# Kernel tuning notes

Measured on AMD Instinct MI355X. Metric: run time of the kernel, lower is better.

The kernel has to match this reference:

```python
import jax, jax.numpy as jnp
import numpy as np

N = 100_000       # nodes
E = 1_600_000     # edges
G = 128           # graphs in batch
RAW_ND, RAW_ED = 9, 3
ND, ED, H = 16, 2, 32  # node_dim, edge_dim, GAT hidden (heads=1)


def _p(key, shape, scale=0.1):
    return jax.random.normal(key, shape, dtype=jnp.float32) * scale


def setup_inputs() -> dict:
    key = jax.random.key(0)
    ks = jax.random.split(key, 32)
    inp = {
        "node_feat": jax.random.normal(ks[0], (N, RAW_ND), dtype=jnp.float32),
        "edge_index": jax.random.randint(ks[1], (2, E), 0, N, dtype=jnp.int64)
        if jax.config.jax_enable_x64 else jax.random.randint(ks[1], (2, E), 0, N).astype(jnp.int32),
        "edge_attr": jax.random.normal(ks[2], (E, RAW_ED), dtype=jnp.float32),
        "batch": jnp.sort(jax.random.randint(ks[3], (N,), 0, G)).astype(jnp.int32),
        # encoders
        "W_ne": _p(ks[4], (RAW_ND, ND)), "b_ne": jnp.zeros((ND,), jnp.float32),
        "W_ee": _p(ks[5], (RAW_ED, ED)), "b_ee": jnp.zeros((ED,), jnp.float32),
        # readout
        "W_l3": _p(ks[6], (3 * H, 1)), "b_l3": jnp.zeros((1,), jnp.float32),
    }
    dims_in = [ND, H, H]
    for i in range(3):
        k = jax.random.split(ks[7 + i], 6)
        inp[f"W{i}"] = _p(k[0], (dims_in[i], H))
        inp[f"as{i}"] = _p(k[1], (H,))
        inp[f"ad{i}"] = _p(k[2], (H,))
        inp[f"We{i}"] = _p(k[3], (ED, H))
        inp[f"ae{i}"] = _p(k[4], (H,))
        inp[f"bb{i}"] = jnp.zeros((H,), jnp.float32)
    return inp


def _segment_softmax(logits, seg, num_segments):
    m = jax.ops.segment_max(logits, seg, num_segments=num_segments)
    m = jnp.where(jnp.isfinite(m), m, 0.0)
    e = jnp.exp(logits - m[seg])
    s = jax.ops.segment_sum(e, seg, num_segments=num_segments)
    return e / (s[seg] + 1e-16)


def _gat(x, src, dst, ef, W, a_s, a_d, We, a_e, b):
    # PyG GATConv, heads=1, negative_slope=0.2
    h = x @ W                                   # [N', H]
    a_src = h @ a_s                             # [N']
    a_dst = h @ a_d
    a_edge = (ef @ We) @ a_e                    # [E']
    logits = jax.nn.leaky_relu(a_src[src] + a_dst[dst] + a_edge, 0.2)
    att = _segment_softmax(logits, dst, h.shape[0])
    out = jax.ops.segment_sum(h[src] * att[:, None], dst, num_segments=h.shape[0])
    return out + b


def reference(node_feat, edge_index, edge_attr, batch,
              W_ne, b_ne, W_ee, b_ee, W_l3, b_l3,
              W0, as0, ad0, We0, ae0, bb0,
              W1, as1, ad1, We1, ae1, bb1,
              W2, as2, ad2, We2, ae2, bb2):
    n = node_feat.shape[0]
    x = node_feat @ W_ne + b_ne                 # NodeEncoder -> [N,16]
    ef = edge_attr @ W_ee + b_ee                # EdgeEncoder -> [E,2]
    # add_self_loops=True with fill_value='mean' (PyG default when edge_dim set)
    loop = jnp.arange(n, dtype=edge_index.dtype)
    src = jnp.concatenate([edge_index[0], loop])
    dst = jnp.concatenate([edge_index[1], loop])
    ef_fill = jnp.broadcast_to(ef.mean(axis=0), (n, ef.shape[1]))
    ef_aug = jnp.concatenate([ef, ef_fill], axis=0)
    x1 = _gat(x, src, dst, ef_aug, W0, as0, ad0, We0, ae0, bb0)
    x2 = _gat(x1, src, dst, ef_aug, W1, as1, ad1, We1, ae1, bb1)
    x3 = _gat(x2, src, dst, ef_aug, W2, as2, ad2, We2, ae2, bb2)
    x_cat = jnp.concatenate([x1, x2, x3], axis=1)  # [N, 96]
    sums = jax.ops.segment_sum(x_cat, batch, num_segments=G)
    cnt = jax.ops.segment_sum(jnp.ones((n,), x_cat.dtype), batch, num_segments=G)
    pooled = sums / jnp.maximum(cnt, 1.0)[:, None]   # global mean pool [G,96]
    return pooled @ W_l3 + b_l3                      # [G,1]
```

## Files before the change

### kernel.cpp

```cpp
#include <hip/hip_runtime.h>
#include <hip/hip_fp16.h>


#define NBUCK_SHIFT 8
#define NBUCK_MAX 512
#define CAP 6144
#define SLF_BIT 0x00800000u

__global__ void k_pre(const int* __restrict__ ei1, int* __restrict__ bucket_cnt,
                      const int* __restrict__ batch, int* __restrict__ bounds,
                      const float* __restrict__ Wne, const float* __restrict__ bne,
                      const float* __restrict__ W0, float* __restrict__ wf,
                      int n, int e, int ep, int nbH) {
    int b = blockIdx.x, t = threadIdx.x;
    if (b < nbH) {
        __shared__ int lh[NBUCK_MAX];
        lh[t] = 0; lh[t + 256] = 0;
        __syncthreads();
        int base = b * 4096;
#pragma unroll
        for (int i = 0; i < 16; ++i) {
            int gid = base + i * 256 + t;
            if (gid < ep) {
                int d = (gid < e) ? ei1[gid] : gid - e;
                atomicAdd(&lh[d >> NBUCK_SHIFT], 1);
            }
        }
        __syncthreads();
        if (lh[t]) atomicAdd(&bucket_cnt[t], lh[t]);
        if (lh[t + 256]) atomicAdd(&bucket_cnt[t + 256], lh[t + 256]);
        return;
    }
    for (int i = t; i < 288; i += 256) {
        int m = i >> 5, j = i & 31;
        float a = 0.f;
        for (int k = 0; k < 16; ++k) a += Wne[m * 16 + k] * W0[k * 32 + j];
        wf[i] = a;
    }
    if (t < 32) {
        float a = 0.f;
        for (int k = 0; k < 16; ++k) a += bne[k] * W0[k * 32 + t];
        wf[288 + t] = a;
    }
    for (int g = t; g <= 128; g += 256) {
        if (g == 128) { bounds[128] = n; continue; }
        int lo = 0, hi = n;
        while (lo < hi) {
            int mid = (lo + hi) >> 1;
            if (batch[mid] < g) lo = mid + 1; else hi = mid;
        }
        bounds[g] = lo;
    }
}

__global__ void k_hproj0(const float* __restrict__ nf, const float* __restrict__ wf,
                         const float* __restrict__ as_, const float* __restrict__ ad_,
                         unsigned int* __restrict__ h2, float* __restrict__ asrc,
                         float* __restrict__ adst, int n) {
    int node = blockIdx.x * 8 + (threadIdx.x >> 5);
    int j = threadIdx.x & 31;
    if (node >= n) return;
    const float* xr = nf + node * 9;
    float acc = wf[288 + j];
#pragma unroll
    for (int m = 0; m < 9; ++m) acc += xr[m] * wf[m * 32 + j];
    float accp = __shfl_down(acc, 1, 32);
    if ((j & 1) == 0) {
        __half2 hh = __floats2half2_rn(acc, accp);
        h2[(size_t)node * 16 + (j >> 1)] = *reinterpret_cast<unsigned int*>(&hh);
    }
    float r1 = acc * as_[j], r2 = acc * ad_[j];
#pragma unroll
    for (int off = 16; off > 0; off >>= 1) {
        r1 += __shfl_xor(r1, off, 32);
        r2 += __shfl_xor(r2, off, 32);
    }
    if (j == 0) { asrc[node] = r1; adst[node] = r2; }
}

__device__ __forceinline__ float2 h2f2u(unsigned int hw) {
    __half2 hh = *reinterpret_cast<__half2*>(&hw);
    return make_float2(__low2float(hh), __high2float(hh));
}

__global__ void k_hproj(const unsigned int* __restrict__ xh, const float* __restrict__ W,
                        const float* __restrict__ as_, const float* __restrict__ ad_,
                        unsigned int* __restrict__ h2, float* __restrict__ asrc,
                        float* __restrict__ adst, int n) {
    __shared__ float sW[1024];
    for (int i = threadIdx.x; i < 1024; i += 256) sW[i] = W[i];
    __syncthreads();
    int node = blockIdx.x * 8 + (threadIdx.x >> 5);
    int j = threadIdx.x & 31;
    if (node >= n) return;
    const unsigned int* xr = xh + (size_t)node * 16;
    float acc = 0.f;
#pragma unroll
    for (int w = 0; w < 16; ++w) {
        float2 f = h2f2u(xr[w]);
        acc += f.x * sW[(2 * w) * 32 + j] + f.y * sW[(2 * w + 1) * 32 + j];
    }
    float accp = __shfl_down(acc, 1, 32);
    if ((j & 1) == 0) {
        __half2 hh = __floats2half2_rn(acc, accp);
        h2[(size_t)node * 16 + (j >> 1)] = *reinterpret_cast<unsigned int*>(&hh);
    }
    float r1 = acc * as_[j], r2 = acc * ad_[j];
#pragma unroll
    for (int off = 16; off > 0; off >>= 1) {
        r1 += __shfl_xor(r1, off, 32);
        r2 += __shfl_xor(r2, off, 32);
    }
    if (j == 0) { asrc[node] = r1; adst[node] = r2; }
}

__global__ void __launch_bounds__(512)
k_scan(const int* __restrict__ bucket_cnt, int* __restrict__ bucket_base,
       int* __restrict__ bcursor, int nbuck, int ep, int* __restrict__ rp, int n) {
    __shared__ int s[512];
    int t = threadIdx.x;
    int v = (t < nbuck) ? bucket_cnt[t] : 0;
    s[t] = v;
    __syncthreads();
    for (int o = 1; o < 512; o <<= 1) {
        int x = (t >= o) ? s[t - o] : 0;
        __syncthreads();
        s[t] += x;
        __syncthreads();
    }
    int ex = s[t] - v;
    if (t < nbuck) { bucket_base[t] = ex; bcursor[t] = ex; }
    if (t == 0) { bucket_base[nbuck] = ep; rp[n] = ep; }
}

__global__ void k_binB(const int* __restrict__ ei0, const int* __restrict__ ei1,
                       const float* __restrict__ ea, const float* __restrict__ We,
                       const float* __restrict__ be, int* __restrict__ bcursor,
                       uint2* __restrict__ st, float2* __restrict__ partial,
                       int e, int ep) {
    __shared__ int lh[NBUCK_MAX], lcur[NBUCK_MAX];
    int t = threadIdx.x;
    lh[t] = 0; lh[t + 256] = 0;
    __syncthreads();
    int base = blockIdx.x * 4096;
    unsigned int sd[16], fh[16];
    int bk[16];
    float w00 = We[0], w10 = We[2], w20 = We[4];
    float w01 = We[1], w11 = We[3], w21 = We[5];
    float b0 = be[0], b1 = be[1];
    float cs0 = 0.f, cs1 = 0.f;
#pragma unroll
    for (int i = 0; i < 16; ++i) {
        int gid = base + i * 256 + t;
        bk[i] = -1;
        if (gid < ep) {
            int s, d;
            if (gid < e) {
                s = ei0[gid]; d = ei1[gid];
                const float* r = ea + (size_t)gid * 3;
                float a0 = r[0], a1 = r[1], a2 = r[2];
                float f0 = a0 * w00 + a1 * w10 + a2 * w20 + b0;
                float f1 = a0 * w01 + a1 * w11 + a2 * w21 + b1;
                cs0 += f0; cs1 += f1;
                sd[i] = ((unsigned int)s << NBUCK_SHIFT) | (unsigned int)(d & 255);
                __half2 hh = __floats2half2_rn(f0, f1);
                fh[i] = *reinterpret_cast<unsigned int*>(&hh);
            } else {
                s = d = gid - e;
                sd[i] = 0x80000000u | ((unsigned int)s << NBUCK_SHIFT)
                      | (unsigned int)(d & 255);
                fh[i] = 0;
            }
            bk[i] = d >> NBUCK_SHIFT;
            atomicAdd(&lh[bk[i]], 1);
        }
    }
#pragma unroll
    for (int off = 32; off > 0; off >>= 1) {
        cs0 += __shfl_xor(cs0, off, 64);
        cs1 += __shfl_xor(cs1, off, 64);
    }
    if ((t & 63) == 0)
        partial[(blockIdx.x << 2) + (t >> 6)] = make_float2(cs0, cs1);
    __syncthreads();
    if (lh[t] > 0) lcur[t] = atomicAdd(&bcursor[t], lh[t]);
    if (lh[t + 256] > 0) lcur[t + 256] = atomicAdd(&bcursor[t + 256], lh[t + 256]);
    __syncthreads();
#pragma unroll
    for (int i = 0; i < 16; ++i) {
        if (bk[i] >= 0) {
            int pos = atomicAdd(&lcur[bk[i]], 1);
            st[pos] = make_uint2(sd[i], fh[i]);
        }
    }
}

__global__ void __launch_bounds__(512)
k_binC(const uint2* __restrict__ st, const int* __restrict__ bucket_base,
       int* __restrict__ rp, uint2* __restrict__ rec, int n, int nbuck,
       const float* __restrict__ We0, const float* __restrict__ ae0,
       const float* __restrict__ We1, const float* __restrict__ ae1,
       const float* __restrict__ We2, const float* __restrict__ ae2,
       const float2* __restrict__ partial, int nw, float einv,
       float* __restrict__ consts) {
    int k = blockIdx.x, t = threadIdx.x;
    if (k == nbuck) {
        __shared__ float r0[512], r1[512];
        float m0 = 0.f, m1 = 0.f;
        for (int i = t; i < nw; i += 512) {
            float2 v = partial[i];
            m0 += v.x; m1 += v.y;
        }
        r0[t] = m0; r1[t] = m1;
        __syncthreads();
        for (int o = 256; o > 0; o >>= 1) {
            if (t < o) { r0[t] += r0[t + o]; r1[t] += r1[t + o]; }
            __syncthreads();
        }
        if (t == 0) {
            float fm0 = r0[0] * einv, fm1 = r1[0] * einv;
            const float* We[3] = {We0, We1, We2};
            const float* ae[3] = {ae0, ae1, ae2};
            for (int l = 0; l < 3; ++l) {
                float c0 = 0.f, c1 = 0.f;
                for (int j = 0; j < 32; ++j) {
                    c0 += We[l][j] * ae[l][j];
                    c1 += We[l][32 + j] * ae[l][j];
                }
                consts[l * 2 + 0] = c0;
                consts[l * 2 + 1] = c1;
                consts[6 + l] = fm0 * c0 + fm1 * c1;
            }
        }
        return;
    }
    __shared__ int nh[256], ns[256];
    __shared__ uint2 rs[CAP];
    int s0 = bucket_base[k], s1 = bucket_base[k + 1];
    int cnt = s1 - s0;
    uint2 lv[12];
    if (t < 256) nh[t] = 0;
    __syncthreads();
#pragma unroll
    for (int u = 0; u < 12; ++u) {
        int i = s0 + u * 512 + t;
        if (i < s1) {
            uint2 v = st[i];
            lv[u] = v;
            atomicAdd(&nh[v.x & 255], 1);
        }
    }
    __syncthreads();
    if (t < 256) ns[t] = nh[t];
    __syncthreads();
    for (int o = 1; o < 256; o <<= 1) {
        int add = 0;
        if (t < 256 && t >= o) add = ns[t - o];
        __syncthreads();
        if (t < 256) ns[t] += add;
        __syncthreads();
    }
    int node0 = k << NBUCK_SHIFT;
    if (t < 256) {
        int startl = ns[t] - nh[t];
        if (node0 + t < n) rp[node0 + t] = s0 + startl;
        nh[t] = startl;
    }
    __syncthreads();
#pragma unroll
    for (int u = 0; u < 12; ++u) {
        int i = s0 + u * 512 + t;
        if (i < s1) {
            uint2 v = lv[u];
            int pos = atomicAdd(&nh[v.x & 255], 1);
            uint2 r = make_uint2(v.x >> NBUCK_SHIFT, v.y);
            if (pos < CAP) rs[pos] = r;
            else rec[s0 + pos] = r;
        }
    }
    __syncthreads();
    int m = cnt < CAP ? cnt : CAP;
    for (int i = t; i < m; i += 512)
        rec[s0 + i] = rs[i];
}

__device__ __forceinline__ void agg_step(const unsigned int* __restrict__ h2,
                                         const uint2* ed, int t, int sub, int woff,
                                         float& a0, float& a1, float& a2, float& a3) {
    uint2 sp = ed[t + sub];
    float p4 = __uint_as_float(sp.y);
    uint2 hv = *reinterpret_cast<const uint2*>(h2 + (((int)sp.x << 4) + woff));
    __half2 hlo = *reinterpret_cast<__half2*>(&hv.x);
    __half2 hhi = *reinterpret_cast<__half2*>(&hv.y);
    a0 = fmaf(__low2float(hlo), p4, a0);
    a1 = fmaf(__high2float(hlo), p4, a1);
    a2 = fmaf(__low2float(hhi), p4, a2);
    a3 = fmaf(__high2float(hhi), p4, a3);
}

template <bool STORE_X>
__global__ void k_agg(const int* __restrict__ rp, const uint2* __restrict__ rec,
                      const float* __restrict__ asrc, const float* __restrict__ adst,
                      const float* __restrict__ consts, const unsigned int* __restrict__ h2,
                      const float* __restrict__ bb, unsigned int* __restrict__ xout,
                      const float* __restrict__ wl3, float* __restrict__ vout,
                      int n, int layer) {
    __shared__ uint2 sed[8][32];
    int g = threadIdx.x >> 5;
    int j = threadIdx.x & 31;
    int sub = j >> 3;
    int q = j & 7;
    int woff = q << 1;
    float c0 = consts[layer * 2], c1 = consts[layer * 2 + 1];
    float loopc = consts[6 + layer];
    float4 bb4 = reinterpret_cast<const float4*>(bb)[q];
    float4 wl34 = reinterpret_cast<const float4*>(wl3)[q];
    uint2* ed = sed[g];
    int stride = gridDim.x * 8;
    for (int node = blockIdx.x * 8 + g; node < n; node += stride) {
        int r0 = rp[node], r1 = rp[node + 1];
        float adn = adst[node];
        float a0 = 0.f, a1 = 0.f, a2 = 0.f, a3 = 0.f, psum = 0.f;
        for (int c = r0; c < r1; c += 32) {
            int i = c + j;
            float pe = 0.f; unsigned int s = 0;
            if (i < r1) {
                unsigned long long rv = __builtin_nontemporal_load(
                    reinterpret_cast<const unsigned long long*>(rec + i));
                unsigned int sx = (unsigned int)rv;
                s = sx & 0x7fffffu;
                unsigned int fv = (unsigned int)(rv >> 32);
                __half2 hh = *reinterpret_cast<__half2*>(&fv);
                float ae = (sx & SLF_BIT) ? loopc
                         : fmaf(__low2float(hh), c0, __high2float(hh) * c1);
                float lg = asrc[s] + adn + ae;
                lg = lg > 0.f ? lg : 0.2f * lg;
                pe = __expf(lg);
            }
            psum += pe;
            ed[j] = make_uint2(s, __float_as_uint(pe));
            int cnt = min(32, r1 - c);
            int t = 0;
            for (; t + 8 <= cnt; t += 8) {
                agg_step(h2, ed, t, sub, woff, a0, a1, a2, a3);
                agg_step(h2, ed, t + 4, sub, woff, a0, a1, a2, a3);
            }
            if (t < cnt) { agg_step(h2, ed, t, sub, woff, a0, a1, a2, a3); t += 4; }
            if (t < cnt) { agg_step(h2, ed, t, sub, woff, a0, a1, a2, a3); }
        }
        a0 += __shfl_xor(a0, 8, 32);  a0 += __shfl_xor(a0, 16, 32);
        a1 += __shfl_xor(a1, 8, 32);  a1 += __shfl_xor(a1, 16, 32);
        a2 += __shfl_xor(a2, 8, 32);  a2 += __shfl_xor(a2, 16, 32);
        a3 += __shfl_xor(a3, 8, 32);  a3 += __shfl_xor(a3, 16, 32);
#pragma unroll
        for (int off = 16; off > 0; off >>= 1) psum += __shfl_xor(psum, off, 32);
        float inv = __builtin_amdgcn_rcpf(psum + 1e-16f);
        float r0v = fmaf(a0, inv, bb4.x);
        float r1v = fmaf(a1, inv, bb4.y);
        float r2v = fmaf(a2, inv, bb4.z);
        float r3v = fmaf(a3, inv, bb4.w);
        if (STORE_X) {
            if (sub == 0) {
                __half2 lo = __floats2half2_rn(r0v, r1v);
                __half2 hi = __floats2half2_rn(r2v, r3v);
                uint2 wv = make_uint2(*reinterpret_cast<unsigned int*>(&lo),
                                      *reinterpret_cast<unsigned int*>(&hi));
                reinterpret_cast<uint2*>(xout)[(size_t)node * 8 + q] = wv;
            }
        }
        float v = r0v * wl34.x + r1v * wl34.y + r2v * wl34.z + r3v * wl34.w;
        v += __shfl_xor(v, 1, 32);
        v += __shfl_xor(v, 2, 32);
        v += __shfl_xor(v, 4, 32);
        if (j == 0) vout[node] = v;
    }
}

__global__ void k_dotv(const float* __restrict__ v0, const float* __restrict__ v1,
                       const float* __restrict__ v2, const int* __restrict__ bounds,
                       const float* __restrict__ bl3, float* __restrict__ out) {
    __shared__ float red[256];
    int g = blockIdx.x, t = threadIdx.x;
    int s0 = bounds[g], s1 = bounds[g + 1];
    float acc = 0.f;
    for (int i = s0 + t; i < s1; i += 256) acc += v0[i] + v1[i] + v2[i];
    red[t] = acc;
    __syncthreads();
    for (int o = 128; o > 0; o >>= 1) {
        if (t < o) red[t] += red[t + o];
        __syncthreads();
    }
    if (t == 0) {
        float c = (float)(s1 - s0);
        if (c < 1.f) c = 1.f;
        out[g] = red[0] / c + bl3[0];
    }
}

extern "C" void kernel_launch(void* const* d_in, const int* in_sizes, int n_in,
                              void* d_out, int out_size, void* d_ws, size_t ws_size,
                              hipStream_t stream) {
    (void)n_in; (void)out_size; (void)ws_size;
    const float* nf    = (const float*)d_in[0];
    const int*   ei    = (const int*)d_in[1];
    const float* ea    = (const float*)d_in[2];
    const int*   batch = (const int*)d_in[3];
    const float* W_ne  = (const float*)d_in[4];
    const float* b_ne  = (const float*)d_in[5];
    const float* W_ee  = (const float*)d_in[6];
    const float* b_ee  = (const float*)d_in[7];
    const float* W_l3  = (const float*)d_in[8];
    const float* b_l3  = (const float*)d_in[9];
    const float *Wl[3], *asl[3], *adl[3], *Wel[3], *ael[3], *bbl[3];
    for (int l = 0; l < 3; ++l) {
        Wl[l]  = (const float*)d_in[10 + 6 * l];
        asl[l] = (const float*)d_in[11 + 6 * l];
        adl[l] = (const float*)d_in[12 + 6 * l];
        Wel[l] = (const float*)d_in[13 + 6 * l];
        ael[l] = (const float*)d_in[14 + 6 * l];
        bbl[l] = (const float*)d_in[15 + 6 * l];
    }

    const int n  = in_sizes[3];
    const int e  = in_sizes[2] / 3;
    const int ep = e + n;
    const int* ei0 = ei;
    const int* ei1 = ei + e;
    const int nbuck = (n + 255) >> NBUCK_SHIFT;

    char* w = (char*)d_ws;
    size_t off = 0;
    auto alloc = [&](size_t b) { size_t o = off; off = (off + b + 255) & ~(size_t)255; return o; };
    unsigned int* x1h     = (unsigned int*)(w + alloc((size_t)n * 16 * 4));
    unsigned int* x2h     = (unsigned int*)(w + alloc((size_t)n * 16 * 4));
    unsigned int* h2a     = (unsigned int*)(w + alloc((size_t)n * 16 * 4));
    unsigned int* h2b     = (unsigned int*)(w + alloc((size_t)n * 16 * 4));
    float*        asrcA   = (float*)(w + alloc((size_t)n * 4));
    float*        adstA   = (float*)(w + alloc((size_t)n * 4));
    float*        asrcB   = (float*)(w + alloc((size_t)n * 4));
    float*        adstB   = (float*)(w + alloc((size_t)n * 4));
    float*        v0      = (float*)(w + alloc((size_t)n * 4));
    float*        v1      = (float*)(w + alloc((size_t)n * 4));
    float*        v2      = (float*)(w + alloc((size_t)n * 4));
    uint2*        st      = (uint2*)(w + alloc((size_t)ep * 8));
    uint2*        rec     = (uint2*)(w + alloc((size_t)ep * 8));
    int*          rp      = (int*)(w + alloc((size_t)(n + 1) * 4));
    int*          bcnt    = (int*)(w + alloc(NBUCK_MAX * 4));
    int*          bbase   = (int*)(w + alloc((NBUCK_MAX + 1) * 4));
    int*          bcur    = (int*)(w + alloc(NBUCK_MAX * 4));
    float2*       partial = (float2*)(w + alloc((size_t)8192 * 8));
    float*        consts  = (float*)(w + alloc(256));
    int*          bounds  = (int*)(w + alloc(129 * 4));
    float*        wfbuf   = (float*)(w + alloc(320 * 4));

    hipMemsetAsync(bcnt, 0, NBUCK_MAX * 4, stream);

    int nbH = (ep + 4095) / 4096;
    int nw  = nbH * 4;
    int nbN = (n + 7) / 8;
    int nbA = 2048;

    k_pre<<<nbH + 1, 256, 0, stream>>>(ei1, bcnt, batch, bounds,
                                       W_ne, b_ne, Wl[0], wfbuf, n, e, ep, nbH);
    k_hproj0<<<nbN, 256, 0, stream>>>(nf, wfbuf, asl[0], adl[0],
                                      h2a, asrcA, adstA, n);
    k_scan<<<1, 512, 0, stream>>>(bcnt, bbase, bcur, nbuck, ep, rp, n);
    k_binB<<<nbH, 256, 0, stream>>>(ei0, ei1, ea, W_ee, b_ee, bcur, st,
                                    partial, e, ep);
    k_binC<<<nbuck + 1, 512, 0, stream>>>(st, bbase, rp, rec, n, nbuck,
                                          Wel[0], ael[0], Wel[1], ael[1],
                                          Wel[2], ael[2], partial, nw,
                                          1.0f / (float)e, consts);

    k_agg<true><<<nbA, 256, 0, stream>>>(rp, rec, asrcA, adstA, consts, h2a,
                                         bbl[0], x1h, W_l3 + 0, v0, n, 0);
    k_hproj<<<nbN, 256, 0, stream>>>(x1h, Wl[1], asl[1], adl[1], h2b, asrcB, adstB, n);
    k_agg<true><<<nbA, 256, 0, stream>>>(rp, rec, asrcB, adstB, consts, h2b,
                                         bbl[1], x2h, W_l3 + 32, v1, n, 1);
    k_hproj<<<nbN, 256, 0, stream>>>(x2h, Wl[2], asl[2], adl[2], h2a, asrcA, adstA, n);
    k_agg<false><<<nbA, 256, 0, stream>>>(rp, rec, asrcA, adstA, consts, h2a,
                                          bbl[2], nullptr, W_l3 + 64, v2, n, 2);
    k_dotv<<<128, 256, 0, stream>>>(v0, v1, v2, bounds, b_l3, (float*)d_out);
}
```

Measured before the change: 316.7 us.

## Fuse next-layer projection into aggregation kernel, drop intermediate x buffers

The aggregation kernel now computes the next layer's linear projection (h = x·W) and its attention source/destination scalars in-register, using shuffles and a shared-memory copy of W. This removes the separate k_hproj launches and the fp16 round trip of x1/x2 through global memory. In exchange, the aggregation kernel uses more shared memory and registers, which may lower occupancy. It also adds 32 shuffles per node. Precision changes slightly because x is no longer rounded to fp16 before the projection.

Result: slower. 329.8 us (+4.1%).

```diff
diff --git a/kernel.cpp b/kernel.cpp
--- a/kernel.cpp
+++ b/kernel.cpp
@@ -64,42 +64,6 @@
     float acc = wf[288 + j];
 #pragma unroll
     for (int m = 0; m < 9; ++m) acc += xr[m] * wf[m * 32 + j];
-    float accp = __shfl_down(acc, 1, 32);
-    if ((j & 1) == 0) {
-        __half2 hh = __floats2half2_rn(acc, accp);
-        h2[(size_t)node * 16 + (j >> 1)] = *reinterpret_cast<unsigned int*>(&hh);
-    }
-    float r1 = acc * as_[j], r2 = acc * ad_[j];
-#pragma unroll
-    for (int off = 16; off > 0; off >>= 1) {
-        r1 += __shfl_xor(r1, off, 32);
-        r2 += __shfl_xor(r2, off, 32);
-    }
-    if (j == 0) { asrc[node] = r1; adst[node] = r2; }
-}
-
-__device__ __forceinline__ float2 h2f2u(unsigned int hw) {
-    __half2 hh = *reinterpret_cast<__half2*>(&hw);
-    return make_float2(__low2float(hh), __high2float(hh));
-}
-
-__global__ void k_hproj(const unsigned int* __restrict__ xh, const float* __restrict__ W,
-                        const float* __restrict__ as_, const float* __restrict__ ad_,
-                        unsigned int* __restrict__ h2, float* __restrict__ asrc,
-                        float* __restrict__ adst, int n) {
-    __shared__ float sW[1024];
-    for (int i = threadIdx.x; i < 1024; i += 256) sW[i] = W[i];
-    __syncthreads();
-    int node = blockIdx.x * 8 + (threadIdx.x >> 5);
-    int j = threadIdx.x & 31;
-    if (node >= n) return;
-    const unsigned int* xr = xh + (size_t)node * 16;
-    float acc = 0.f;
-#pragma unroll
-    for (int w = 0; w < 16; ++w) {
-        float2 f = h2f2u(xr[w]);
-        acc += f.x * sW[(2 * w) * 32 + j] + f.y * sW[(2 * w + 1) * 32 + j];
-    }
     float accp = __shfl_down(acc, 1, 32);
     if ((j & 1) == 0) {
         __half2 hh = __floats2half2_rn(acc, accp);
@@ -298,16 +262,25 @@
     a3 = fmaf(__high2float(hhi), p4, a3);
 }
 
-template <bool STORE_X>
+template <bool PROJ>
 __global__ void k_agg(const int* __restrict__ rp, const uint2* __restrict__ rec,
                       const float* __restrict__ asrc, const float* __restrict__ adst,
                       const float* __restrict__ consts, const unsigned int* __restrict__ h2,
-                      const float* __restrict__ bb, unsigned int* __restrict__ xout,
+                      const float* __restrict__ bb,
                       const float* __restrict__ wl3, float* __restrict__ vout,
+                      const float* __restrict__ Wn, const float* __restrict__ asn,
+                      const float* __restrict__ adn_,
+                      unsigned int* __restrict__ h2out, float* __restrict__ asrcO,
+                      float* __restrict__ adstO,
                       int n, int layer) {
     __shared__ uint2 sed[8][32];
+    __shared__ float sW[1024];
     int g = threadIdx.x >> 5;
     int j = threadIdx.x & 31;
+    if (PROJ) {
+        for (int i = threadIdx.x; i < 1024; i += 256) sW[i] = Wn[i];
+        __syncthreads();
+    }
     int sub = j >> 3;
     int q = j & 7;
     int woff = q << 1;
@@ -315,6 +288,8 @@
     float loopc = consts[6 + layer];
     float4 bb4 = reinterpret_cast<const float4*>(bb)[q];
     float4 wl34 = reinterpret_cast<const float4*>(wl3)[q];
+    float asj = PROJ ? asn[j] : 0.f;
+    float adj = PROJ ? adn_[j] : 0.f;
     uint2* ed = sed[g];
     int stride = gridDim.x * 8;
     for (int node = blockIdx.x * 8 + g; node < n; node += stride) {
@@ -355,24 +330,42 @@
 #pragma unroll
         for (int off = 16; off > 0; off >>= 1) psum += __shfl_xor(psum, off, 32);
         float inv = __builtin_amdgcn_rcpf(psum + 1e-16f);
-        float r0v = fmaf(a0, inv, bb4.x);
-        float r1v = fmaf(a1, inv, bb4.y);
-        float r2v = fmaf(a2, inv, bb4.z);
-        float r3v = fmaf(a3, inv, bb4.w);
-        if (STORE_X) {
-            if (sub == 0) {
-                __half2 lo = __floats2half2_rn(r0v, r1v);
-                __half2 hi = __floats2half2_rn(r2v, r3v);
-                uint2 wv = make_uint2(*reinterpret_cast<unsigned int*>(&lo),
-                                      *reinterpret_cast<unsigned int*>(&hi));
-                reinterpret_cast<uint2*>(xout)[(size_t)node * 8 + q] = wv;
-            }
-        }
-        float v = r0v * wl34.x + r1v * wl34.y + r2v * wl34.z + r3v * wl34.w;
+        float xq0 = fmaf(a0, inv, bb4.x);
+        float xq1 = fmaf(a1, inv, bb4.y);
+        float xq2 = fmaf(a2, inv, bb4.z);
+        float xq3 = fmaf(a3, inv, bb4.w);
+        float v = xq0 * wl34.x + xq1 * wl34.y + xq2 * wl34.z + xq3 * wl34.w;
         v += __shfl_xor(v, 1, 32);
         v += __shfl_xor(v, 2, 32);
         v += __shfl_xor(v, 4, 32);
         if (j == 0) vout[node] = v;
+        if (PROJ) {
+            float h = 0.f;
+#pragma unroll
+            for (int k = 0; k < 32; ++k) {
+                float xk;
+                switch (k & 3) {
+                    case 0: xk = __shfl(xq0, k >> 2, 32); break;
+                    case 1: xk = __shfl(xq1, k >> 2, 32); break;
+                    case 2: xk = __shfl(xq2, k >> 2, 32); break;
+                    default: xk = __shfl(xq3, k >> 2, 32); break;
+                }
+                h = fmaf(xk, sW[k * 32 + j], h);
+            }
+            float hp = __shfl_down(h, 1, 32);
+            if ((j & 1) == 0) {
+                __half2 hh = __floats2half2_rn(h, hp);
+                h2out[(size_t)node * 16 + (j >> 1)] =
+                    *reinterpret_cast<unsigned int*>(&hh);
+            }
+            float r1v = h * asj, r2v = h * adj;
+#pragma unroll
+            for (int off = 16; off > 0; off >>= 1) {
+                r1v += __shfl_xor(r1v, off, 32);
+                r2v += __shfl_xor(r2v, off, 32);
+            }
+            if (j == 0) { asrcO[node] = r1v; adstO[node] = r2v; }
+        }
     }
 }
 
@@ -431,8 +424,6 @@
     char* w = (char*)d_ws;
     size_t off = 0;
     auto alloc = [&](size_t b) { size_t o = off; off = (off + b + 255) & ~(size_t)255; return o; };
-    unsigned int* x1h     = (unsigned int*)(w + alloc((size_t)n * 16 * 4));
-    unsigned int* x2h     = (unsigned int*)(w + alloc((size_t)n * 16 * 4));
     unsigned int* h2a     = (unsigned int*)(w + alloc((size_t)n * 16 * 4));
     unsigned int* h2b     = (unsigned int*)(w + alloc((size_t)n * 16 * 4));
     float*        asrcA   = (float*)(w + alloc((size_t)n * 4));
@@ -473,12 +464,16 @@
                                           1.0f / (float)e, consts);
 
     k_agg<true><<<nbA, 256, 0, stream>>>(rp, rec, asrcA, adstA, consts, h2a,
-                                         bbl[0], x1h, W_l3 + 0, v0, n, 0);
-    k_hproj<<<nbN, 256, 0, stream>>>(x1h, Wl[1], asl[1], adl[1], h2b, asrcB, adstB, n);
+                                         bbl[0], W_l3 + 0, v0,
+                                         Wl[1], asl[1], adl[1],
+                                         h2b, asrcB, adstB, n, 0);
     k_agg<true><<<nbA, 256, 0, stream>>>(rp, rec, asrcB, adstB, consts, h2b,
-                                         bbl[1], x2h, W_l3 + 32, v1, n, 1);
-    k_hproj<<<nbN, 256, 0, stream>>>(x2h, Wl[2], asl[2], adl[2], h2a, asrcA, adstA, n);
+                                         bbl[1], W_l3 + 32, v1,
+                                         Wl[2], asl[2], adl[2],
+                                         h2a, asrcA, adstA, n, 1);
     k_agg<false><<<nbA, 256, 0, stream>>>(rp, rec, asrcA, adstA, consts, h2a,
-                                          bbl[2], nullptr, W_l3 + 64, v2, n, 2);
+                                          bbl[2], W_l3 + 64, v2,
+                                          nullptr, nullptr, nullptr,
+                                          nullptr, nullptr, nullptr, n, 2);
     k_dotv<<<128, 256, 0, stream>>>(v0, v1, v2, bounds, b_l3, (float*)d_out);
 }
```

## Interleave two destination nodes per 32-lane group in GAT aggregation

Applied to the files above, without the earlier changes.

Each 32-lane group in k_agg now handles two adjacent destination nodes together. Their edge records, attention logits and gathered h rows are loaded and accumulated in the same loop, with separate shared-memory staging buffers, to raise memory-level parallelism and hide gather latency. The cost is more registers per thread, clamped extra loads for lanes past a node's edge range, and divergence when the two nodes have different degrees.

Result: slower. 331.2 us (+4.6%).

```diff
diff --git a/kernel.cpp b/kernel.cpp
--- a/kernel.cpp
+++ b/kernel.cpp
@@ -298,6 +298,21 @@
     a3 = fmaf(__high2float(hhi), p4, a3);
 }
 
+__device__ __forceinline__ void decode_pe(unsigned long long rv, float asv,
+                                          float adn, float c0, float c1,
+                                          float loopc, bool valid,
+                                          unsigned int& s, float& pe) {
+    unsigned int sx = (unsigned int)rv;
+    s = sx & 0x7fffffu;
+    unsigned int fv = (unsigned int)(rv >> 32);
+    __half2 hh = *reinterpret_cast<__half2*>(&fv);
+    float ae = (sx & SLF_BIT) ? loopc
+             : fmaf(__low2float(hh), c0, __high2float(hh) * c1);
+    float lg = asv + adn + ae;
+    lg = lg > 0.f ? lg : 0.2f * lg;
+    pe = valid ? __expf(lg) : 0.f;
+}
+
 template <bool STORE_X>
 __global__ void k_agg(const int* __restrict__ rp, const uint2* __restrict__ rec,
                       const float* __restrict__ asrc, const float* __restrict__ adst,
@@ -305,7 +320,7 @@
                       const float* __restrict__ bb, unsigned int* __restrict__ xout,
                       const float* __restrict__ wl3, float* __restrict__ vout,
                       int n, int layer) {
-    __shared__ uint2 sed[8][32];
+    __shared__ uint2 sed[8][2][32];
     int g = threadIdx.x >> 5;
     int j = threadIdx.x & 31;
     int sub = j >> 3;
@@ -315,64 +330,94 @@
     float loopc = consts[6 + layer];
     float4 bb4 = reinterpret_cast<const float4*>(bb)[q];
     float4 wl34 = reinterpret_cast<const float4*>(wl3)[q];
-    uint2* ed = sed[g];
-    int stride = gridDim.x * 8;
-    for (int node = blockIdx.x * 8 + g; node < n; node += stride) {
-        int r0 = rp[node], r1 = rp[node + 1];
-        float adn = adst[node];
-        float a0 = 0.f, a1 = 0.f, a2 = 0.f, a3 = 0.f, psum = 0.f;
-        for (int c = r0; c < r1; c += 32) {
-            int i = c + j;
-            float pe = 0.f; unsigned int s = 0;
-            if (i < r1) {
-                unsigned long long rv = __builtin_nontemporal_load(
-                    reinterpret_cast<const unsigned long long*>(rec + i));
-                unsigned int sx = (unsigned int)rv;
-                s = sx & 0x7fffffu;
-                unsigned int fv = (unsigned int)(rv >> 32);
-                __half2 hh = *reinterpret_cast<__half2*>(&fv);
-                float ae = (sx & SLF_BIT) ? loopc
-                         : fmaf(__low2float(hh), c0, __high2float(hh) * c1);
-                float lg = asrc[s] + adn + ae;
-                lg = lg > 0.f ? lg : 0.2f * lg;
-                pe = __expf(lg);
+    uint2* edA = sed[g][0];
+    uint2* edB = sed[g][1];
+    int stride = gridDim.x * 16;
+    for (int nA = (blockIdx.x * 8 + g) * 2; nA < n; nA += stride) {
+        int nB = nA + 1;
+        bool hasB = nB < n;
+        int rA0 = rp[nA], rA1 = rp[nA + 1];
+        int rB0 = rA1, rB1 = hasB ? rp[nA + 2] : rA1;
+        float adA = adst[nA];
+        float adB = hasB ? adst[nB] : 0.f;
+        float aA0 = 0.f, aA1 = 0.f, aA2 = 0.f, aA3 = 0.f, psA = 0.f;
+        float aB0 = 0.f, aB1 = 0.f, aB2 = 0.f, aB3 = 0.f, psB = 0.f;
+        int cA = rA0, cB = rB0;
+        while (cA < rA1 || cB < rB1) {
+            int iA = cA + j, iB = cB + j;
+            bool vA = iA < rA1, vB = iB < rB1;
+            int liA = vA ? iA : rA1 - 1;
+            int liB = vB ? iB : (rB1 > rB0 ? rB1 - 1 : rA1 - 1);
+            unsigned long long rvA = __builtin_nontemporal_load(
+                reinterpret_cast<const unsigned long long*>(rec + liA));
+            unsigned long long rvB = __builtin_nontemporal_load(
+                reinterpret_cast<const unsigned long long*>(rec + liB));
+            unsigned int sA, sB;
+            float peA, peB;
+            decode_pe(rvA, asrc[(unsigned int)rvA & 0x7fffffu], adA,
+                      c0, c1, loopc, vA, sA, peA);
+            decode_pe(rvB, asrc[(unsigned int)rvB & 0x7fffffu], adB,
+                      c0, c1, loopc, vB, sB, peB);
+            psA += peA; psB += peB;
+            edA[j] = make_uint2(sA, __float_as_uint(peA));
+            edB[j] = make_uint2(sB, __float_as_uint(peB));
+            int cntA = rA1 - cA; cntA = cntA < 0 ? 0 : (cntA > 32 ? 32 : cntA);
+            int cntB = rB1 - cB; cntB = cntB < 0 ? 0 : (cntB > 32 ? 32 : cntB);
+            int cm = cntA > cntB ? cntA : cntB;
+            for (int t = 0; t < cm; t += 4) {
+                if (t < cntA) agg_step(h2, edA, t, sub, woff, aA0, aA1, aA2, aA3);
+                if (t < cntB) agg_step(h2, edB, t, sub, woff, aB0, aB1, aB2, aB3);
             }
-            psum += pe;
-            ed[j] = make_uint2(s, __float_as_uint(pe));
-            int cnt = min(32, r1 - c);
-            int t = 0;
-            for (; t + 8 <= cnt; t += 8) {
-                agg_step(h2, ed, t, sub, woff, a0, a1, a2, a3);
-                agg_step(h2, ed, t + 4, sub, woff, a0, a1, a2, a3);
-            }
-            if (t < cnt) { agg_step(h2, ed, t, sub, woff, a0, a1, a2, a3); t += 4; }
-            if (t < cnt) { agg_step(h2, ed, t, sub, woff, a0, a1, a2, a3); }
-        }
-        a0 += __shfl_xor(a0, 8, 32);  a0 += __shfl_xor(a0, 16, 32);
-        a1 += __shfl_xor(a1, 8, 32);  a1 += __shfl_xor(a1, 16, 32);
-        a2 += __shfl_xor(a2, 8, 32);  a2 += __shfl_xor(a2, 16, 32);
-        a3 += __shfl_xor(a3, 8, 32);  a3 += __shfl_xor(a3, 16, 32);
-#pragma unroll
-        for (int off = 16; off > 0; off >>= 1) psum += __shfl_xor(psum, off, 32);
-        float inv = __builtin_amdgcn_rcpf(psum + 1e-16f);
-        float r0v = fmaf(a0, inv, bb4.x);
-        float r1v = fmaf(a1, inv, bb4.y);
-        float r2v = fmaf(a2, inv, bb4.z);
-        float r3v = fmaf(a3, inv, bb4.w);
-        if (STORE_X) {
-            if (sub == 0) {
-                __half2 lo = __floats2half2_rn(r0v, r1v);
-                __half2 hi = __floats2half2_rn(r2v, r3v);
+            cA += 32; cB += 32;
+        }
+        aA0 += __shfl_xor(aA0, 8, 32);  aA0 += __shfl_xor(aA0, 16, 32);
+        aA1 += __shfl_xor(aA1, 8, 32);  aA1 += __shfl_xor(aA1, 16, 32);
+        aA2 += __shfl_xor(aA2, 8, 32);  aA2 += __shfl_xor(aA2, 16, 32);
+        aA3 += __shfl_xor(aA3, 8, 32);  aA3 += __shfl_xor(aA3, 16, 32);
+#pragma unroll
+        for (int off = 16; off > 0; off >>= 1) psA += __shfl_xor(psA, off, 32);
+        float invA = __builtin_amdgcn_rcpf(psA + 1e-16f);
+        float xA0 = fmaf(aA0, invA, bb4.x);
+        float xA1 = fmaf(aA1, invA, bb4.y);
+        float xA2 = fmaf(aA2, invA, bb4.z);
+        float xA3 = fmaf(aA3, invA, bb4.w);
+        if (STORE_X && sub == 0) {
+            __half2 lo = __floats2half2_rn(xA0, xA1);
+            __half2 hi = __floats2half2_rn(xA2, xA3);
+            uint2 wv = make_uint2(*reinterpret_cast<unsigned int*>(&lo),
+                                  *reinterpret_cast<unsigned int*>(&hi));
+            reinterpret_cast<uint2*>(xout)[(size_t)nA * 8 + q] = wv;
+        }
+        float vA = xA0 * wl34.x + xA1 * wl34.y + xA2 * wl34.z + xA3 * wl34.w;
+        vA += __shfl_xor(vA, 1, 32);
+        vA += __shfl_xor(vA, 2, 32);
+        vA += __shfl_xor(vA, 4, 32);
+        if (j == 0) vout[nA] = vA;
+        if (hasB) {
+            aB0 += __shfl_xor(aB0, 8, 32);  aB0 += __shfl_xor(aB0, 16, 32);
+            aB1 += __shfl_xor(aB1, 8, 32);  aB1 += __shfl_xor(aB1, 16, 32);
+            aB2 += __shfl_xor(aB2, 8, 32);  aB2 += __shfl_xor(aB2, 16, 32);
+            aB3 += __shfl_xor(aB3, 8, 32);  aB3 += __shfl_xor(aB3, 16, 32);
+#pragma unroll
+            for (int off = 16; off > 0; off >>= 1) psB += __shfl_xor(psB, off, 32);
+            float invB = __builtin_amdgcn_rcpf(psB + 1e-16f);
+            float xB0 = fmaf(aB0, invB, bb4.x);
+            float xB1 = fmaf(aB1, invB, bb4.y);
+            float xB2 = fmaf(aB2, invB, bb4.z);
+            float xB3 = fmaf(aB3, invB, bb4.w);
+            if (STORE_X && sub == 0) {
+                __half2 lo = __floats2half2_rn(xB0, xB1);
+                __half2 hi = __floats2half2_rn(xB2, xB3);
                 uint2 wv = make_uint2(*reinterpret_cast<unsigned int*>(&lo),
                                       *reinterpret_cast<unsigned int*>(&hi));
-                reinterpret_cast<uint2*>(xout)[(size_t)node * 8 + q] = wv;
+                reinterpret_cast<uint2*>(xout)[(size_t)nB * 8 + q] = wv;
             }
-        }
-        float v = r0v * wl34.x + r1v * wl34.y + r2v * wl34.z + r3v * wl34.w;
-        v += __shfl_xor(v, 1, 32);
-        v += __shfl_xor(v, 2, 32);
-        v += __shfl_xor(v, 4, 32);
-        if (j == 0) vout[node] = v;
+            float vB = xB0 * wl34.x + xB1 * wl34.y + xB2 * wl34.z + xB3 * wl34.w;
+            vB += __shfl_xor(vB, 1, 32);
+            vB += __shfl_xor(vB, 2, 32);
+            vB += __shfl_xor(vB, 4, 32);
+            if (j == 0) vout[nB] = vB;
+        }
     }
 }
 
```

## Replace two-pass bucket sort with per-node degree count and direct CSR scatter

Applied to the files above, without the earlier changes.

The edge binning is rebuilt. Instead of a coarse bucket histogram, a staging buffer and a per-bucket local sort in shared memory, the code now counts per-node in-degree with global atomics. It builds row pointers with a per-bucket scan and scatters each edge record straight to its final CSR slot through a per-node atomic cursor. This removes the staging buffer pass and the shared-memory sort kernel, but adds global atomics per edge on the degree and cursor arrays and leaves record order within a node nondeterministic. The self-loop flag encoding also changes to SLF_BIT, on the assumption that the aggregation kernel expects this layout.

Result: slower. 474.1 us (+49.7%).

```diff
diff --git a/kernel.cpp b/kernel.cpp
--- a/kernel.cpp
+++ b/kernel.cpp
@@ -4,14 +4,14 @@
 
 #define NBUCK_SHIFT 8
 #define NBUCK_MAX 512
-#define CAP 6144
 #define SLF_BIT 0x00800000u
 
 __global__ void k_pre(const int* __restrict__ ei1, int* __restrict__ bucket_cnt,
+                      int* __restrict__ deg,
                       const int* __restrict__ batch, int* __restrict__ bounds,
                       const float* __restrict__ Wne, const float* __restrict__ bne,
                       const float* __restrict__ W0, float* __restrict__ wf,
-                      int n, int e, int ep, int nbH) {
+                      int n, int e, int nbH) {
     int b = blockIdx.x, t = threadIdx.x;
     if (b < nbH) {
         __shared__ int lh[NBUCK_MAX];
@@ -21,9 +21,10 @@
 #pragma unroll
         for (int i = 0; i < 16; ++i) {
             int gid = base + i * 256 + t;
-            if (gid < ep) {
-                int d = (gid < e) ? ei1[gid] : gid - e;
+            if (gid < e) {
+                int d = ei1[gid];
                 atomicAdd(&lh[d >> NBUCK_SHIFT], 1);
+                atomicAdd(&deg[d], 1);
             }
         }
         __syncthreads();
@@ -116,10 +117,15 @@
 
 __global__ void __launch_bounds__(512)
 k_scan(const int* __restrict__ bucket_cnt, int* __restrict__ bucket_base,
-       int* __restrict__ bcursor, int nbuck, int ep, int* __restrict__ rp, int n) {
+       int nbuck, int ep, int* __restrict__ rp, int n) {
     __shared__ int s[512];
     int t = threadIdx.x;
-    int v = (t < nbuck) ? bucket_cnt[t] : 0;
+    int v = 0;
+    if (t < nbuck) {
+        int rem = n - (t << NBUCK_SHIFT);
+        int nodes = rem > 256 ? 256 : (rem > 0 ? rem : 0);
+        v = bucket_cnt[t] + nodes;
+    }
     s[t] = v;
     __syncthreads();
     for (int o = 1; o < 512; o <<= 1) {
@@ -129,22 +135,38 @@
         __syncthreads();
     }
     int ex = s[t] - v;
-    if (t < nbuck) { bucket_base[t] = ex; bcursor[t] = ex; }
+    if (t < nbuck) bucket_base[t] = ex;
     if (t == 0) { bucket_base[nbuck] = ep; rp[n] = ep; }
 }
 
-__global__ void k_binB(const int* __restrict__ ei0, const int* __restrict__ ei1,
-                       const float* __restrict__ ea, const float* __restrict__ We,
-                       const float* __restrict__ be, int* __restrict__ bcursor,
-                       uint2* __restrict__ st, float2* __restrict__ partial,
-                       int e, int ep) {
-    __shared__ int lh[NBUCK_MAX], lcur[NBUCK_MAX];
+__global__ void k_rp(const int* __restrict__ deg, const int* __restrict__ bucket_base,
+                     int* __restrict__ rp, int* __restrict__ cursor, int n) {
+    __shared__ int s[256];
+    int k = blockIdx.x, t = threadIdx.x;
+    int node = (k << NBUCK_SHIFT) + t;
+    int v = (node < n) ? deg[node] + 1 : 0;
+    s[t] = v;
+    __syncthreads();
+    for (int o = 1; o < 256; o <<= 1) {
+        int x = (t >= o) ? s[t - o] : 0;
+        __syncthreads();
+        s[t] += x;
+        __syncthreads();
+    }
+    if (node < n) {
+        int pos = bucket_base[k] + s[t] - v;
+        rp[node] = pos;
+        cursor[node] = pos;
+    }
+}
+
+__global__ void k_bin(const int* __restrict__ ei0, const int* __restrict__ ei1,
+                      const float* __restrict__ ea, const float* __restrict__ We,
+                      const float* __restrict__ be, int* __restrict__ cursor,
+                      uint2* __restrict__ rec, float2* __restrict__ partial,
+                      int e, int ep) {
     int t = threadIdx.x;
-    lh[t] = 0; lh[t + 256] = 0;
-    __syncthreads();
     int base = blockIdx.x * 4096;
-    unsigned int sd[16], fh[16];
-    int bk[16];
     float w00 = We[0], w10 = We[2], w20 = We[4];
     float w01 = We[1], w11 = We[3], w21 = We[5];
     float b0 = be[0], b1 = be[1];
@@ -152,27 +174,26 @@
 #pragma unroll
     for (int i = 0; i < 16; ++i) {
         int gid = base + i * 256 + t;
-        bk[i] = -1;
         if (gid < ep) {
-            int s, d;
+            unsigned int sx, fh;
+            int d;
             if (gid < e) {
-                s = ei0[gid]; d = ei1[gid];
+                int s = ei0[gid]; d = ei1[gid];
                 const float* r = ea + (size_t)gid * 3;
                 float a0 = r[0], a1 = r[1], a2 = r[2];
-                float f0 = a0 * w00 + a1 * w10 + a2 * w20 + b0;
-                float f1 = a0 * w01 + a1 * w11 + a2 * w21 + b1;
+                float f0 = fmaf(a0, w00, fmaf(a1, w10, fmaf(a2, w20, b0)));
+                float f1 = fmaf(a0, w01, fmaf(a1, w11, fmaf(a2, w21, b1)));
                 cs0 += f0; cs1 += f1;
-                sd[i] = ((unsigned int)s << NBUCK_SHIFT) | (unsigned int)(d & 255);
                 __half2 hh = __floats2half2_rn(f0, f1);
-                fh[i] = *reinterpret_cast<unsigned int*>(&hh);
+                fh = *reinterpret_cast<unsigned int*>(&hh);
+                sx = (unsigned int)s;
             } else {
-                s = d = gid - e;
-                sd[i] = 0x80000000u | ((unsigned int)s << NBUCK_SHIFT)
-                      | (unsigned int)(d & 255);
-                fh[i] = 0;
-            }
-            bk[i] = d >> NBUCK_SHIFT;
-            atomicAdd(&lh[bk[i]], 1);
+                d = gid - e;
+                sx = (unsigned int)d | SLF_BIT;
+                fh = 0;
+            }
+            int pos = atomicAdd(&cursor[d], 1);
+            rec[pos] = make_uint2(sx, fh);
         }
     }
 #pragma unroll
@@ -182,106 +203,42 @@
     }
     if ((t & 63) == 0)
         partial[(blockIdx.x << 2) + (t >> 6)] = make_float2(cs0, cs1);
+}
+
+__global__ void __launch_bounds__(512)
+k_consts(const float2* __restrict__ partial, int nw, float einv,
+         const float* __restrict__ We0, const float* __restrict__ ae0,
+         const float* __restrict__ We1, const float* __restrict__ ae1,
+         const float* __restrict__ We2, const float* __restrict__ ae2,
+         float* __restrict__ consts) {
+    __shared__ float r0[512], r1[512];
+    int t = threadIdx.x;
+    float m0 = 0.f, m1 = 0.f;
+    for (int i = t; i < nw; i += 512) {
+        float2 v = partial[i];
+        m0 += v.x; m1 += v.y;
+    }
+    r0[t] = m0; r1[t] = m1;
     __syncthreads();
-    if (lh[t] > 0) lcur[t] = atomicAdd(&bcursor[t], lh[t]);
-    if (lh[t + 256] > 0) lcur[t + 256] = atomicAdd(&bcursor[t + 256], lh[t + 256]);
-    __syncthreads();
-#pragma unroll
-    for (int i = 0; i < 16; ++i) {
-        if (bk[i] >= 0) {
-            int pos = atomicAdd(&lcur[bk[i]], 1);
-            st[pos] = make_uint2(sd[i], fh[i]);
-        }
-    }
-}
-
-__global__ void __launch_bounds__(512)
-k_binC(const uint2* __restrict__ st, const int* __restrict__ bucket_base,
-       int* __restrict__ rp, uint2* __restrict__ rec, int n, int nbuck,
-       const float* __restrict__ We0, const float* __restrict__ ae0,
-       const float* __restrict__ We1, const float* __restrict__ ae1,
-       const float* __restrict__ We2, const float* __restrict__ ae2,
-       const float2* __restrict__ partial, int nw, float einv,
-       float* __restrict__ consts) {
-    int k = blockIdx.x, t = threadIdx.x;
-    if (k == nbuck) {
-        __shared__ float r0[512], r1[512];
-        float m0 = 0.f, m1 = 0.f;
-        for (int i = t; i < nw; i += 512) {
-            float2 v = partial[i];
-            m0 += v.x; m1 += v.y;
-        }
-        r0[t] = m0; r1[t] = m1;
-        __syncthreads();
-        for (int o = 256; o > 0; o >>= 1) {
-            if (t < o) { r0[t] += r0[t + o]; r1[t] += r1[t + o]; }
-            __syncthreads();
-        }
-        if (t == 0) {
-            float fm0 = r0[0] * einv, fm1 = r1[0] * einv;
-            const float* We[3] = {We0, We1, We2};
-            const float* ae[3] = {ae0, ae1, ae2};
-            for (int l = 0; l < 3; ++l) {
-                float c0 = 0.f, c1 = 0.f;
-                for (int j = 0; j < 32; ++j) {
-                    c0 += We[l][j] * ae[l][j];
-                    c1 += We[l][32 + j] * ae[l][j];
-                }
-                consts[l * 2 + 0] = c0;
-                consts[l * 2 + 1] = c1;
-                consts[6 + l] = fm0 * c0 + fm1 * c1;
-            }
-        }
-        return;
-    }
-    __shared__ int nh[256], ns[256];
-    __shared__ uint2 rs[CAP];
-    int s0 = bucket_base[k], s1 = bucket_base[k + 1];
-    int cnt = s1 - s0;
-    uint2 lv[12];
-    if (t < 256) nh[t] = 0;
-    __syncthreads();
-#pragma unroll
-    for (int u = 0; u < 12; ++u) {
-        int i = s0 + u * 512 + t;
-        if (i < s1) {
-            uint2 v = st[i];
-            lv[u] = v;
-            atomicAdd(&nh[v.x & 255], 1);
-        }
-    }
-    __syncthreads();
-    if (t < 256) ns[t] = nh[t];
-    __syncthreads();
-    for (int o = 1; o < 256; o <<= 1) {
-        int add = 0;
-        if (t < 256 && t >= o) add = ns[t - o];
-        __syncthreads();
-        if (t < 256) ns[t] += add;
-        __syncthreads();
-    }
-    int node0 = k << NBUCK_SHIFT;
-    if (t < 256) {
-        int startl = ns[t] - nh[t];
-        if (node0 + t < n) rp[node0 + t] = s0 + startl;
-        nh[t] = startl;
-    }
-    __syncthreads();
-#pragma unroll
-    for (int u = 0; u < 12; ++u) {
-        int i = s0 + u * 512 + t;
-        if (i < s1) {
-            uint2 v = lv[u];
-            int pos = atomicAdd(&nh[v.x & 255], 1);
-            uint2 r = make_uint2(v.x >> NBUCK_SHIFT, v.y);
-            if (pos < CAP) rs[pos] = r;
-            else rec[s0 + pos] = r;
-        }
-    }
-    __syncthreads();
-    int m = cnt < CAP ? cnt : CAP;
-    for (int i = t; i < m; i += 512)
-        rec[s0 + i] = rs[i];
+    for (int o = 256; o > 0; o >>= 1) {
+        if (t < o) { r0[t] += r0[t + o]; r1[t] += r1[t + o]; }
+        __syncthreads();
+    }
+    if (t == 0) {
+        float fm0 = r0[0] * einv, fm1 = r1[0] * einv;
+        const float* We[3] = {We0, We1, We2};
+        const float* ae[3] = {ae0, ae1, ae2};
+        for (int l = 0; l < 3; ++l) {
+            float c0 = 0.f, c1 = 0.f;
+            for (int j = 0; j < 32; ++j) {
+                c0 += We[l][j] * ae[l][j];
+                c1 += We[l][32 + j] * ae[l][j];
+            }
+            consts[l * 2 + 0] = c0;
+            consts[l * 2 + 1] = c1;
+            consts[6 + l] = fm0 * c0 + fm1 * c1;
+        }
+    }
 }
 
 __device__ __forceinline__ void agg_step(const unsigned int* __restrict__ h2,
@@ -442,35 +399,36 @@
     float*        v0      = (float*)(w + alloc((size_t)n * 4));
     float*        v1      = (float*)(w + alloc((size_t)n * 4));
     float*        v2      = (float*)(w + alloc((size_t)n * 4));
-    uint2*        st      = (uint2*)(w + alloc((size_t)ep * 8));
     uint2*        rec     = (uint2*)(w + alloc((size_t)ep * 8));
     int*          rp      = (int*)(w + alloc((size_t)(n + 1) * 4));
+    int*          deg     = (int*)(w + alloc((size_t)n * 4));
+    int*          cursor  = (int*)(w + alloc((size_t)n * 4));
     int*          bcnt    = (int*)(w + alloc(NBUCK_MAX * 4));
     int*          bbase   = (int*)(w + alloc((NBUCK_MAX + 1) * 4));
-    int*          bcur    = (int*)(w + alloc(NBUCK_MAX * 4));
     float2*       partial = (float2*)(w + alloc((size_t)8192 * 8));
     float*        consts  = (float*)(w + alloc(256));
     int*          bounds  = (int*)(w + alloc(129 * 4));
     float*        wfbuf   = (float*)(w + alloc(320 * 4));
 
     hipMemsetAsync(bcnt, 0, NBUCK_MAX * 4, stream);
+    hipMemsetAsync(deg, 0, (size_t)n * 4, stream);
 
     int nbH = (ep + 4095) / 4096;
     int nw  = nbH * 4;
     int nbN = (n + 7) / 8;
     int nbA = 2048;
 
-    k_pre<<<nbH + 1, 256, 0, stream>>>(ei1, bcnt, batch, bounds,
-                                       W_ne, b_ne, Wl[0], wfbuf, n, e, ep, nbH);
+    k_pre<<<nbH + 1, 256, 0, stream>>>(ei1, bcnt, deg, batch, bounds,
+                                       W_ne, b_ne, Wl[0], wfbuf, n, e, nbH);
     k_hproj0<<<nbN, 256, 0, stream>>>(nf, wfbuf, asl[0], adl[0],
                                       h2a, asrcA, adstA, n);
-    k_scan<<<1, 512, 0, stream>>>(bcnt, bbase, bcur, nbuck, ep, rp, n);
-    k_binB<<<nbH, 256, 0, stream>>>(ei0, ei1, ea, W_ee, b_ee, bcur, st,
-                                    partial, e, ep);
-    k_binC<<<nbuck + 1, 512, 0, stream>>>(st, bbase, rp, rec, n, nbuck,
-                                          Wel[0], ael[0], Wel[1], ael[1],
-                                          Wel[2], ael[2], partial, nw,
-                                          1.0f / (float)e, consts);
+    k_scan<<<1, 512, 0, stream>>>(bcnt, bbase, nbuck, ep, rp, n);
+    k_rp<<<nbuck, 256, 0, stream>>>(deg, bbase, rp, cursor, n);
+    k_bin<<<nbH, 256, 0, stream>>>(ei0, ei1, ea, W_ee, b_ee, cursor,
+                                   rec, partial, e, ep);
+    k_consts<<<1, 512, 0, stream>>>(partial, nw, 1.0f / (float)e,
+                                    Wel[0], ael[0], Wel[1], ael[1],
+                                    Wel[2], ael[2], consts);
 
     k_agg<true><<<nbA, 256, 0, stream>>>(rp, rec, asrcA, adstA, consts, h2a,
                                          bbl[0], x1h, W_l3 + 0, v0, n, 0);
```
